# Kernel optimization log

Hardware: AMD Instinct MI355X
Metric: run time of the kernel (lower is better)

The kernel has to match this reference:

```python
import jax, jax.numpy as jnp
import numpy as np

N_QUBITS = 6
N_LAYERS = 2
QSVT_DEGREE = 3
BATCH = 128
SEQ_LEN = 512
DIM = 2 ** N_QUBITS
# wire 0 is the most-significant bit in the statevector index (PennyLane convention)
_POP = np.array([bin(i).count('1') for i in range(DIM)], dtype=np.float32)
PHASE_SIGN = jnp.asarray(N_QUBITS - 2.0 * _POP)  # (DIM,): sum_w (1 - 2*bit_w)


def _rx(t):
    c = jnp.cos(0.5 * t).astype(jnp.complex64)
    s = (-1j * jnp.sin(0.5 * t)).astype(jnp.complex64)
    return jnp.stack([jnp.stack([c, s]), jnp.stack([s, c])])


def _ry(t):
    c = jnp.cos(0.5 * t).astype(jnp.complex64)
    s = jnp.sin(0.5 * t).astype(jnp.complex64)
    return jnp.stack([jnp.stack([c, -s]), jnp.stack([s, c])])


def _rz(t):
    e = jnp.exp(-0.5j * t.astype(jnp.complex64))
    z = jnp.zeros((), jnp.complex64)
    return jnp.stack([jnp.stack([e, z]), jnp.stack([z, jnp.conj(e)])])


def _apply_1q(psi, U, w):
    # psi: (B,) + (2,)*N_QUBITS ; U: (2,2) complex, same for all batch elems
    psi = jnp.moveaxis(psi, 1 + w, -1)
    psi = psi @ U.T
    return jnp.moveaxis(psi, -1, 1 + w)


def _apply_ry_batched(psi, theta, w):
    # RY with a per-batch angle theta: (B,)
    psi = jnp.moveaxis(psi, 1 + w, -1)
    c = jnp.cos(0.5 * theta).reshape((-1,) + (1,) * (N_QUBITS - 1))
    s = jnp.sin(0.5 * theta).reshape((-1,) + (1,) * (N_QUBITS - 1))
    a, b = psi[..., 0], psi[..., 1]
    psi = jnp.stack([c * a - s * b, s * a + c * b], axis=-1)
    return jnp.moveaxis(psi, -1, 1 + w)


def _cnot(psi, c, t):
    p0 = jax.lax.index_in_dim(psi, 0, axis=1 + c, keepdims=True)
    p1 = jax.lax.index_in_dim(psi, 1, axis=1 + c, keepdims=True)
    p1 = jnp.flip(p1, axis=1 + t)
    return jnp.concatenate([p0, p1], axis=1 + c)


def _circuit_step(h, x, params, poly):
    # h, x: (B, N_QUBITS) angles. Returns <Z_w> per qubit: (B, N_QUBITS).
    B = h.shape[0]
    # 1) state encoding: RY(h_w)|0> = cos(h/2)|0> + sin(h/2)|1>  (product state)
    c, s = jnp.cos(0.5 * h), jnp.sin(0.5 * h)
    psi = jnp.ones((B, 1), jnp.complex64)
    for w in range(N_QUBITS):
        amp = jnp.stack([c[:, w], s[:, w]], axis=-1).astype(jnp.complex64)  # (B,2)
        psi = (psi[:, :, None] * amp[:, None, :]).reshape(B, -1)
    psi = psi.reshape((B,) + (2,) * N_QUBITS)
    # 2) QSVT block: RZ(coeff*pi) on every wire fuses into one diagonal phase
    for d in range(QSVT_DEGREE + 1):
        theta = poly[d] * np.pi
        phase = jnp.exp((-0.5j) * theta * PHASE_SIGN)  # (DIM,)
        psi = (psi.reshape(B, -1) * phase[None, :]).reshape((B,) + (2,) * N_QUBITS)
        for i in range(N_QUBITS - 1):
            psi = _cnot(psi, i, i + 1)
        psi = _cnot(psi, N_QUBITS - 1, 0)  # ring closure
    # 3) variational layers: per-wire RZ@RY@RX (RX applied first), then CNOT chain
    idx = 0
    for _ in range(N_LAYERS):
        for i in range(N_QUBITS):
            U = _rz(params[idx + 2]) @ _ry(params[idx + 1]) @ _rx(params[idx])
            psi = _apply_1q(psi, U, i)
            idx += 3
        for i in range(N_QUBITS - 1):
            psi = _cnot(psi, i, i + 1)
    # 4) input injection: RY(x_w) with per-batch angles
    for w in range(N_QUBITS):
        psi = _apply_ry_batched(psi, x[:, w], w)
    # 5) measurement: <Z_w> = P(bit_w=0) - P(bit_w=1)
    p = jnp.abs(psi) ** 2
    zs = []
    for w in range(N_QUBITS):
        axes = tuple(a for a in range(1, N_QUBITS + 1) if a != 1 + w)
        pw = p.sum(axis=axes)  # (B,2)
        zs.append(pw[:, 0] - pw[:, 1])
    return jnp.stack(zs, axis=-1)


def _ssm_pass(angles, params, poly, reverse):
    a = jnp.flip(angles, axis=1) if reverse else angles
    xs = jnp.moveaxis(a, 1, 0)  # (T, B, n)
    h0 = jnp.zeros((a.shape[0], N_QUBITS), jnp.float32)

    def step(h, x):
        hn = _circuit_step(h, x, params, poly)
        return hn, hn

    _, ys = jax.lax.scan(step, h0, xs)
    out = jnp.moveaxis(ys, 0, 1)  # (B, T, n)
    return jnp.flip(out, axis=1) if reverse else out


def setup_inputs() -> dict:
    key = jax.random.key(0)
    k0, k1, k2, k3 = jax.random.split(key, 4)
    angles = jax.random.uniform(k0, (BATCH, SEQ_LEN, N_QUBITS), jnp.float32) * np.float32(np.pi)
    poly_coeffs = jax.random.normal(k1, (QSVT_DEGREE + 1,), jnp.float32) * 0.1
    fwd_params = jax.random.normal(k2, (N_QUBITS * N_LAYERS * 3,), jnp.float32) * 0.1
    bwd_params = jax.random.normal(k3, (N_QUBITS * N_LAYERS * 3,), jnp.float32) * 0.1
    fwd_coeff = jnp.full((1,), 0.5, jnp.float32)
    bwd_coeff = jnp.full((1,), 0.5, jnp.float32)
    return {'angles': angles, 'poly_coeffs': poly_coeffs, 'fwd_params': fwd_params,
            'bwd_params': bwd_params, 'fwd_coeff': fwd_coeff, 'bwd_coeff': bwd_coeff}


def reference(angles, poly_coeffs, fwd_params, bwd_params, fwd_coeff, bwd_coeff):
    h_fwd = _ssm_pass(angles, fwd_params, poly_coeffs, reverse=False)
    h_bwd = _ssm_pass(angles, bwd_params, poly_coeffs, reverse=True)
    return jax.nn.sigmoid(fwd_coeff) * h_fwd + jax.nn.sigmoid(bwd_coeff) * h_bwd
```

## Files before the change

kernel.cpp:

```cpp
#include <hip/hip_runtime.h>
#include <hip/hip_bf16.h>
#include <stdint.h>

#define BATCH 128
#define SEQ   512
#define NW    6
#define DIM   64
#define NELEM (BATCH * SEQ * NW)
#define PI_F  3.14159265358979323846f

typedef float v2f __attribute__((ext_vector_type(2)));
typedef uint16_t u16x8 __attribute__((ext_vector_type(8)));

__device__ __forceinline__ v2f pkfma(float s, v2f m, v2f a) {
    return __builtin_elementwise_fma((v2f){s, s}, m, a);
}

template <int CTRL>
__device__ __forceinline__ float dpp_add(float v) {
    return v + __int_as_float(__builtin_amdgcn_update_dpp(
        0, __float_as_int(v), CTRL, 0xF, 0xF, true));
}

template <int CTRL>
__device__ __forceinline__ void red6(float v[6]) {
#pragma unroll
    for (int k = 0; k < 6; ++k) v[k] = dpp_add<CTRL>(v[k]);
}

template <int CTRL>
__device__ __forceinline__ float dpp_mov(float x) {
    return __int_as_float(__builtin_amdgcn_update_dpp(
        0, __float_as_int(x), CTRL, 0xF, 0xF, true));
}

__device__ __forceinline__ float ldf(const void* p, int i, bool bf) {
    if (bf) {
        uint32_t u = (uint32_t)((const uint16_t*)p)[i];
        return __uint_as_float(u << 16);
    }
    return ((const float*)p)[i];
}

__global__ void k_prep(const void* ang, const void* poly, const void* fp,
                       const void* bp, const void* fc, const void* bc,
                       float* __restrict__ misc, float* __restrict__ Mg,
                       int* __restrict__ flag) {
    __shared__ int cnt;
    if (threadIdx.x == 0) cnt = 0;
    __syncthreads();
    {
        uint32_t w = ((const uint32_t*)ang)[threadIdx.x & 255];
        uint32_t e = (w >> 8) & 0xFFu;
        if (e >= 0x3Au && e <= 0x41u) atomicAdd(&cnt, 1);
    }
    __syncthreads();
    const bool bf = (cnt >= 128);

    if (blockIdx.x == 32) {
        if (threadIdx.x == 0)      misc[76] = ldf(fc, 0, bf);
        else if (threadIdx.x == 1) misc[77] = ldf(bc, 0, bf);
        else if (threadIdx.x == 2) *flag = bf ? 1 : 0;
        return;
    }

    const int lane = threadIdx.x & 63;
    const int tix  = blockIdx.x * 4 + (threadIdx.x >> 6);
    const int dir  = tix >> 6;
    const int col  = tix & 63;
    const void* prm = dir ? bp : fp;
    const int p = lane;

    float yr = (p == col) ? 1.f : 0.f;
    float yi = 0.f;

#pragma unroll
    for (int d = 0; d < 4; ++d) {
        const float th = 0.5f * PI_F * ldf(poly, d, bf) *
                         (float)(6 - 2 * (int)__popc((unsigned)p));
        float s, c;
        __sincosf(th, &s, &c);
        const float nr = yr * c + yi * s;
        const float ni = yi * c - yr * s;
        yr = nr; yi = ni;
#pragma unroll
        for (int k = 0; k < 6; ++k) {
            const int cw = k, tw = (k + 1) % 6;
            const int src = p ^ (((p >> (5 - cw)) & 1) << (5 - tw));
            yr = __shfl(yr, src, 64);
            yi = __shfl(yi, src, 64);
        }
    }

    int idx = 0;
#pragma unroll
    for (int l = 0; l < 2; ++l) {
#pragma unroll
        for (int w = 0; w < 6; ++w) {
            float cx, sx, cy, sy, cz, sz;
            __sincosf(0.5f * ldf(prm, idx + 0, bf), &sx, &cx);
            __sincosf(0.5f * ldf(prm, idx + 1, bf), &sy, &cy);
            __sincosf(0.5f * ldf(prm, idx + 2, bf), &sz, &cz);
            idx += 3;
            const float A = cy * cx, B = sy * sx, C = sy * cx, D = cy * sx;
            const float U00r = cz * A + sz * B, U00i = cz * B - sz * A;
            const float U11r = U00r,            U11i = sz * A - cz * B;
            const float Xr   = cz * C + sz * D, Xi   = sz * C - cz * D;
            const int m  = 1 << (5 - w);
            const int bb = (p >> (5 - w)) & 1;
            const float C1r = bb ? U11r : U00r;
            const float C1i = bb ? U11i : U00i;
            const float C2r = bb ? Xr : -Xr;
            const float C2i = Xi;
            const float pr = __shfl_xor(yr, m, 64);
            const float pi = __shfl_xor(yi, m, 64);
            const float nr = C1r * yr - C1i * yi + C2r * pr - C2i * pi;
            const float ni = C1r * yi + C1i * yr + C2r * pi + C2i * pr;
            yr = nr; yi = ni;
        }
#pragma unroll
        for (int k = 0; k < 5; ++k) {
            const int src = p ^ (((p >> (5 - k)) & 1) << (5 - (k + 1)));
            yr = __shfl(yr, src, 64);
            yi = __shfl(yi, src, 64);
        }
    }

    float* out = Mg + ((size_t)(dir * 64 + p) * 64 + (size_t)col) * 2;
    out[0] = yr;
    out[1] = yi;
}

__global__ void __launch_bounds__(128, 1) k_sim(const void* __restrict__ ang,
                                                const float* __restrict__ Mg,
                                                float* __restrict__ hbuf,
                                                const int* __restrict__ flag) {
    const int tid   = threadIdx.x;
    const int lane  = tid & 63;
    const int wv    = tid >> 6;
    const int chain = blockIdx.x;
    const int dir   = chain >> 7;
    const int b     = chain & 127;
    const bool bf   = (*flag != 0);

    __shared__ __align__(16) float  cl[SEQ * 12];
    __shared__ __align__(16) float  zb[SEQ * NW];
    __shared__ float2 pY[2][2][DIM];

    if (!bf) {
        const float4* src =
            (const float4*)((const float*)ang + (size_t)b * (SEQ * NW));
#pragma unroll
        for (int k = 0; k < 6; ++k) {
            const int v = k * 128 + tid;
            const float4 a = src[v];
            __align__(16) float o[8];
            float s, c;
            __sincosf(a.x, &s, &c); o[0] = c; o[1] = s;
            __sincosf(a.y, &s, &c); o[2] = c; o[3] = s;
            __sincosf(a.z, &s, &c); o[4] = c; o[5] = s;
            __sincosf(a.w, &s, &c); o[6] = c; o[7] = s;
            ((float4*)cl)[2 * v]     = ((const float4*)o)[0];
            ((float4*)cl)[2 * v + 1] = ((const float4*)o)[1];
        }
    } else {
        const u16x8* src =
            (const u16x8*)((const uint16_t*)ang + (size_t)b * (SEQ * NW));
#pragma unroll
        for (int k = 0; k < 3; ++k) {
            const int v = k * 128 + tid;
            const u16x8 a = src[v];
            __align__(16) float o[16];
#pragma unroll
            for (int e = 0; e < 8; ++e) {
                const float x = __uint_as_float(((uint32_t)a[e]) << 16);
                float s, c;
                __sincosf(x, &s, &c);
                o[2 * e] = c; o[2 * e + 1] = s;
            }
#pragma unroll
            for (int j = 0; j < 4; ++j)
                ((float4*)cl)[4 * v + j] = ((const float4*)o)[j];
        }
    }

    v2f Mres[32];
    {
        const float2* mr2 =
            (const float2*)(Mg + (size_t)(dir * 64 + lane) * 128 + 64 * wv);
#pragma unroll
        for (int k = 0; k < 32; ++k) Mres[k] = (v2f){mr2[k].x, mr2[k].y};
    }

    int zmask[6];
#pragma unroll
    for (int w = 0; w < 6; ++w) zmask[w] = ((lane >> (5 - w)) & 1) << 31;
    const int ow = wv ^ 1;

    float h[6] = {0.f, 0.f, 0.f, 0.f, 0.f, 0.f};

    auto encode_matvec = [&](v2f& acc) {
        const v2f kc1 = {2.6041667e-3f, 2.6041667e-3f};
        const v2f kc0 = {-0.125f, -0.125f};
        const v2f ks1 = {2.6041667e-4f, 2.6041667e-4f};
        const v2f ks0 = {-2.0833333e-2f, -2.0833333e-2f};
        const v2f one = {1.f, 1.f}, half = {0.5f, 0.5f};
        v2f hp0 = {h[0], h[1]}, hp1 = {h[2], h[3]}, hp2 = {h[4], h[5]};
        v2f u0 = hp0 * hp0, u1 = hp1 * hp1, u2 = hp2 * hp2;
        v2f c0 = __builtin_elementwise_fma(u0,
                    __builtin_elementwise_fma(u0, kc1, kc0), one);
        v2f c1 = __builtin_elementwise_fma(u1,
                    __builtin_elementwise_fma(u1, kc1, kc0), one);
        v2f c2 = __builtin_elementwise_fma(u2,
                    __builtin_elementwise_fma(u2, kc1, kc0), one);
        v2f s0 = hp0 * __builtin_elementwise_fma(u0,
                    __builtin_elementwise_fma(u0, ks1, ks0), half);
        v2f s1 = hp1 * __builtin_elementwise_fma(u1,
                    __builtin_elementwise_fma(u1, ks1, ks0), half);
        v2f s2 = hp2 * __builtin_elementwise_fma(u2,
                    __builtin_elementwise_fma(u2, ks1, ks0), half);
        const float t0 = wv ? s0.x : c0.x;
        const float gA = t0 * c0.y, gB = t0 * s0.y;
        float eH4[4];
        eH4[0] = gA * c1.x; eH4[1] = gA * s1.x;
        eH4[2] = gB * c1.x; eH4[3] = gB * s1.x;
        float g45[4], eL[8];
        g45[0] = c2.x * c2.y; g45[1] = c2.x * s2.y;
        g45[2] = s2.x * c2.y; g45[3] = s2.x * s2.y;
#pragma unroll
        for (int j = 0; j < 8; ++j)
            eL[j] = ((j >> 2) ? s1.y : c1.y) * g45[j & 3];
        v2f y = {0.f, 0.f};
#pragma unroll
        for (int a = 0; a < 4; ++a) {
            v2f T = {0.f, 0.f};
#pragma unroll
            for (int jl = 0; jl < 8; ++jl)
                T = pkfma(eL[jl], Mres[8 * a + jl], T);
            y = pkfma(eH4[a], T, y);
        }
        acc = y;
    };

    const float* cp = cl + (dir ? (SEQ - 1) * 12 : 0);
    const int   cstep = dir ? -12 : 12;
    float*       zp = zb + (dir ? (SEQ - 1) * NW : 0);
    const int   zstep = dir ? -NW : NW;

    __syncthreads();

    v2f myacc;
    encode_matvec(myacc);
    pY[0][wv][lane] = (float2){myacc.x, myacc.y};
    float4 xq0 = ((const float4*)cp)[0];
    float4 xq1 = ((const float4*)cp)[1];
    float4 xq2 = ((const float4*)cp)[2];
    cp += cstep;
    __syncthreads();

    for (int t = 0; t < SEQ; ++t) {
        const int buf = t & 1;

        const float2 yP = pY[buf][ow][lane];
        const float yr = myacc.x + yP.x;
        const float yi = myacc.y + yP.y;
        const int yri = __float_as_int(yr), yii = __float_as_int(yi);

        float dot[6];
        {
            auto rr = __builtin_amdgcn_permlane32_swap(yri, yri, false, false);
            auto ri = __builtin_amdgcn_permlane32_swap(yii, yii, false, false);
            dot[0] = fmaf(__int_as_float((int)rr[0]), __int_as_float((int)rr[1]),
                          __int_as_float((int)ri[0]) * __int_as_float((int)ri[1]));
        }
        {
            auto rr = __builtin_amdgcn_permlane16_swap(yri, yri, false, false);
            auto ri = __builtin_amdgcn_permlane16_swap(yii, yii, false, false);
            dot[1] = fmaf(__int_as_float((int)rr[0]), __int_as_float((int)rr[1]),
                          __int_as_float((int)ri[0]) * __int_as_float((int)ri[1]));
        }
        dot[2] = fmaf(yr, dpp_mov<0x128>(yr), yi * dpp_mov<0x128>(yi));
        dot[3] = fmaf(yr, dpp_mov<0x141>(dpp_mov<0x1B>(yr)),
                      yi * dpp_mov<0x141>(dpp_mov<0x1B>(yi)));
        dot[4] = fmaf(yr, dpp_mov<0x4E>(yr), yi * dpp_mov<0x4E>(yi));
        dot[5] = fmaf(yr, dpp_mov<0xB1>(yr), yi * dpp_mov<0xB1>(yi));

        const float q = fmaf(yr, yr, yi * yi);
        const float cx[6] = {xq0.x, xq0.z, xq1.x, xq1.z, xq2.x, xq2.z};
        const float sx[6] = {xq0.y, xq0.w, xq1.y, xq1.w, xq2.y, xq2.w};

        float v[6];
#pragma unroll
        for (int w = 0; w < 6; ++w) {
            const float cq = __int_as_float(__float_as_int(cx[w] * q) ^ zmask[w]);
            v[w] = fmaf(-sx[w], dot[w], cq);
        }

        if (t + 1 < SEQ) {
            xq0 = ((const float4*)cp)[0];
            xq1 = ((const float4*)cp)[1];
            xq2 = ((const float4*)cp)[2];
            cp += cstep;
        }

        red6<0x111>(v);
        red6<0x112>(v);
        red6<0x114>(v);
        red6<0x118>(v);
        red6<0x142>(v);
        red6<0x143>(v);

        if (tid == 63) {
#pragma unroll
            for (int w = 0; w < 6; ++w) zp[w] = v[w];
        }
        zp += zstep;
#pragma unroll
        for (int w = 0; w < 6; ++w)
            h[w] = __int_as_float(
                __builtin_amdgcn_readlane(__float_as_int(v[w]), 63));

        encode_matvec(myacc);
        pY[buf ^ 1][wv][lane] = (float2){myacc.x, myacc.y};
        __syncthreads();
    }

    {
        const float4* zs4 = (const float4*)zb;
        float4* go = (float4*)(hbuf + (size_t)dir * NELEM +
                               (size_t)b * (SEQ * NW));
#pragma unroll
        for (int k = 0; k < 6; ++k) {
            const int idx = tid + k * 128;
            go[idx] = zs4[idx];
        }
    }
}

__global__ void k_combine(const float* __restrict__ hbuf,
                          const float* __restrict__ misc,
                          void* __restrict__ out, const int* __restrict__ flag) {
    const int i = blockIdx.x * blockDim.x + threadIdx.x;
    if (i >= NELEM) return;
    const float sf = 1.f / (1.f + __expf(-misc[76]));
    const float sb = 1.f / (1.f + __expf(-misc[77]));
    const float v = sf * hbuf[i] + sb * hbuf[NELEM + i];
    if (*flag) ((__hip_bfloat16*)out)[i] = __float2bfloat16(v);
    else       ((float*)out)[i] = v;
}

extern "C" void kernel_launch(void* const* d_in, const int* in_sizes, int n_in,
                              void* d_out, int out_size, void* d_ws, size_t ws_size,
                              hipStream_t stream) {
    const void* ang  = d_in[0];
    const void* poly = d_in[1];
    const void* fp   = d_in[2];
    const void* bp   = d_in[3];
    const void* fc   = d_in[4];
    const void* bc   = d_in[5];

    float* misc = (float*)d_ws + 32;
    float* hbuf = misc + 128;
    float* Mg   = hbuf + 2 * NELEM;
    int*   flag = (int*)(Mg + 2 * 64 * 64 * 2);

    k_prep<<<33, 256, 0, stream>>>(ang, poly, fp, bp, fc, bc, misc, Mg, flag);
    k_sim<<<256, 128, 0, stream>>>(ang, Mg, hbuf, flag);
    k_combine<<<(NELEM + 255) / 256, 256, 0, stream>>>(hbuf, misc, d_out, flag);
}
```

Before: 360.0 us.

## Split complex matvec by real/imag across waves, exchange reduced expectations only

Each of the two waves now holds either the real or the imaginary rows of the circuit matrix over the full 64-column input, instead of half the columns of both parts. Each wave therefore computes one complete component of the output amplitude. The per-lane partial-sum exchange through LDS is replaced by an exchange of only the six reduced per-qubit values, which are summed to give the next hidden state. This removes the 64-entry pY buffer traffic and the packed real/imag arithmetic in the dot products. In exchange, both waves must compute the full encoding products and the barrier now sits between the reduction and the next step's matvec, which may serialize the recurrence more.

Measured after the change: 379.2 us. 5.3% more time.

```diff
diff --git a/kernel.cpp b/kernel.cpp
--- a/kernel.cpp
+++ b/kernel.cpp
@@ -44,7 +44,7 @@
 
 __global__ void k_prep(const void* ang, const void* poly, const void* fp,
                        const void* bp, const void* fc, const void* bc,
-                       float* __restrict__ misc, float* __restrict__ Mg,
+                       float* __restrict__ misc, float* __restrict__ Mgc,
                        int* __restrict__ flag) {
     __shared__ int cnt;
     if (threadIdx.x == 0) cnt = 0;
@@ -126,13 +126,14 @@
         }
     }
 
-    float* out = Mg + ((size_t)(dir * 64 + p) * 64 + (size_t)col) * 2;
-    out[0] = yr;
-    out[1] = yi;
+    const int jh = col >> 3, jl = col & 7;
+    const int off = ((jh >> 1) * 8 + jl) * 2 + (jh & 1);
+    Mgc[((size_t)(dir * 2 + 0) * 64 + p) * 64 + off] = yr;
+    Mgc[((size_t)(dir * 2 + 1) * 64 + p) * 64 + off] = yi;
 }
 
 __global__ void __launch_bounds__(128, 1) k_sim(const void* __restrict__ ang,
-                                                const float* __restrict__ Mg,
+                                                const float* __restrict__ Mgc,
                                                 float* __restrict__ hbuf,
                                                 const int* __restrict__ flag) {
     const int tid   = threadIdx.x;
@@ -145,7 +146,7 @@
 
     __shared__ __align__(16) float  cl[SEQ * 12];
     __shared__ __align__(16) float  zb[SEQ * NW];
-    __shared__ float2 pY[2][2][DIM];
+    __shared__ __align__(16) float  tot[2][2][8];
 
     if (!bf) {
         const float4* src =
@@ -184,123 +185,112 @@
         }
     }
 
-    v2f Mres[32];
+    v2f Mv[32];
     {
-        const float2* mr2 =
-            (const float2*)(Mg + (size_t)(dir * 64 + lane) * 128 + 64 * wv);
-#pragma unroll
-        for (int k = 0; k < 32; ++k) Mres[k] = (v2f){mr2[k].x, mr2[k].y};
+        const float4* mr4 =
+            (const float4*)(Mgc + ((size_t)(dir * 2 + wv) * 64 + lane) * 64);
+#pragma unroll
+        for (int k = 0; k < 16; ++k) {
+            const float4 m = mr4[k];
+            Mv[2 * k]     = (v2f){m.x, m.y};
+            Mv[2 * k + 1] = (v2f){m.z, m.w};
+        }
     }
 
     int zmask[6];
 #pragma unroll
     for (int w = 0; w < 6; ++w) zmask[w] = ((lane >> (5 - w)) & 1) << 31;
-    const int ow = wv ^ 1;
-
-    float h[6] = {0.f, 0.f, 0.f, 0.f, 0.f, 0.f};
-
-    auto encode_matvec = [&](v2f& acc) {
-        const v2f kc1 = {2.6041667e-3f, 2.6041667e-3f};
-        const v2f kc0 = {-0.125f, -0.125f};
-        const v2f ks1 = {2.6041667e-4f, 2.6041667e-4f};
-        const v2f ks0 = {-2.0833333e-2f, -2.0833333e-2f};
-        const v2f one = {1.f, 1.f}, half = {0.5f, 0.5f};
-        v2f hp0 = {h[0], h[1]}, hp1 = {h[2], h[3]}, hp2 = {h[4], h[5]};
-        v2f u0 = hp0 * hp0, u1 = hp1 * hp1, u2 = hp2 * hp2;
-        v2f c0 = __builtin_elementwise_fma(u0,
-                    __builtin_elementwise_fma(u0, kc1, kc0), one);
-        v2f c1 = __builtin_elementwise_fma(u1,
-                    __builtin_elementwise_fma(u1, kc1, kc0), one);
-        v2f c2 = __builtin_elementwise_fma(u2,
-                    __builtin_elementwise_fma(u2, kc1, kc0), one);
-        v2f s0 = hp0 * __builtin_elementwise_fma(u0,
-                    __builtin_elementwise_fma(u0, ks1, ks0), half);
-        v2f s1 = hp1 * __builtin_elementwise_fma(u1,
-                    __builtin_elementwise_fma(u1, ks1, ks0), half);
-        v2f s2 = hp2 * __builtin_elementwise_fma(u2,
-                    __builtin_elementwise_fma(u2, ks1, ks0), half);
-        const float t0 = wv ? s0.x : c0.x;
-        const float gA = t0 * c0.y, gB = t0 * s0.y;
-        float eH4[4];
-        eH4[0] = gA * c1.x; eH4[1] = gA * s1.x;
-        eH4[2] = gB * c1.x; eH4[3] = gB * s1.x;
-        float g45[4], eL[8];
-        g45[0] = c2.x * c2.y; g45[1] = c2.x * s2.y;
-        g45[2] = s2.x * c2.y; g45[3] = s2.x * s2.y;
-#pragma unroll
-        for (int j = 0; j < 8; ++j)
-            eL[j] = ((j >> 2) ? s1.y : c1.y) * g45[j & 3];
-        v2f y = {0.f, 0.f};
-#pragma unroll
-        for (int a = 0; a < 4; ++a) {
-            v2f T = {0.f, 0.f};
-#pragma unroll
-            for (int jl = 0; jl < 8; ++jl)
-                T = pkfma(eL[jl], Mres[8 * a + jl], T);
-            y = pkfma(eH4[a], T, y);
-        }
-        acc = y;
-    };
 
     const float* cp = cl + (dir ? (SEQ - 1) * 12 : 0);
     const int   cstep = dir ? -12 : 12;
     float*       zp = zb + (dir ? (SEQ - 1) * NW : 0);
     const int   zstep = dir ? -NW : NW;
 
-    __syncthreads();
-
-    v2f myacc;
-    encode_matvec(myacc);
-    pY[0][wv][lane] = (float2){myacc.x, myacc.y};
-    float4 xq0 = ((const float4*)cp)[0];
-    float4 xq1 = ((const float4*)cp)[1];
-    float4 xq2 = ((const float4*)cp)[2];
-    cp += cstep;
+    float h[6] = {0.f, 0.f, 0.f, 0.f, 0.f, 0.f};
+
     __syncthreads();
 
     for (int t = 0; t < SEQ; ++t) {
         const int buf = t & 1;
 
-        const float2 yP = pY[buf][ow][lane];
-        const float yr = myacc.x + yP.x;
-        const float yi = myacc.y + yP.y;
-        const int yri = __float_as_int(yr), yii = __float_as_int(yi);
-
-        float dot[6];
+        const float4 xq0 = ((const float4*)cp)[0];
+        const float4 xq1 = ((const float4*)cp)[1];
+        const float4 xq2 = ((const float4*)cp)[2];
+        cp += cstep;
+
+        float cw[6], sw[6];
         {
-            auto rr = __builtin_amdgcn_permlane32_swap(yri, yri, false, false);
-            auto ri = __builtin_amdgcn_permlane32_swap(yii, yii, false, false);
-            dot[0] = fmaf(__int_as_float((int)rr[0]), __int_as_float((int)rr[1]),
-                          __int_as_float((int)ri[0]) * __int_as_float((int)ri[1]));
-        }
+            const v2f kc1 = {2.6041667e-3f, 2.6041667e-3f};
+            const v2f kc0 = {-0.125f, -0.125f};
+            const v2f ks1 = {2.6041667e-4f, 2.6041667e-4f};
+            const v2f ks0 = {-2.0833333e-2f, -2.0833333e-2f};
+            const v2f one = {1.f, 1.f}, half = {0.5f, 0.5f};
+            v2f hp0 = {h[0], h[1]}, hp1 = {h[2], h[3]}, hp2 = {h[4], h[5]};
+            v2f u0 = hp0 * hp0, u1 = hp1 * hp1, u2 = hp2 * hp2;
+            v2f c0 = __builtin_elementwise_fma(u0,
+                        __builtin_elementwise_fma(u0, kc1, kc0), one);
+            v2f c1 = __builtin_elementwise_fma(u1,
+                        __builtin_elementwise_fma(u1, kc1, kc0), one);
+            v2f c2 = __builtin_elementwise_fma(u2,
+                        __builtin_elementwise_fma(u2, kc1, kc0), one);
+            v2f s0 = hp0 * __builtin_elementwise_fma(u0,
+                        __builtin_elementwise_fma(u0, ks1, ks0), half);
+            v2f s1 = hp1 * __builtin_elementwise_fma(u1,
+                        __builtin_elementwise_fma(u1, ks1, ks0), half);
+            v2f s2 = hp2 * __builtin_elementwise_fma(u2,
+                        __builtin_elementwise_fma(u2, ks1, ks0), half);
+            cw[0] = c0.x; cw[1] = c0.y; cw[2] = c1.x; cw[3] = c1.y;
+            cw[4] = c2.x; cw[5] = c2.y;
+            sw[0] = s0.x; sw[1] = s0.y; sw[2] = s1.x; sw[3] = s1.y;
+            sw[4] = s2.x; sw[5] = s2.y;
+        }
+
+        float g01[4], g45[4], eH[8], eL[8];
+        g01[0] = cw[0] * cw[1]; g01[1] = cw[0] * sw[1];
+        g01[2] = sw[0] * cw[1]; g01[3] = sw[0] * sw[1];
+        g45[0] = cw[4] * cw[5]; g45[1] = cw[4] * sw[5];
+        g45[2] = sw[4] * cw[5]; g45[3] = sw[4] * sw[5];
+#pragma unroll
+        for (int j = 0; j < 8; ++j) {
+            eH[j] = g01[j >> 1] * ((j & 1) ? sw[2] : cw[2]);
+            eL[j] = ((j >> 2) ? sw[3] : cw[3]) * g45[j & 3];
+        }
+
+        float yc = 0.f;
+#pragma unroll
+        for (int p2 = 0; p2 < 4; ++p2) {
+            v2f T = {0.f, 0.f};
+#pragma unroll
+            for (int jl = 0; jl < 8; ++jl)
+                T = pkfma(eL[jl], Mv[8 * p2 + jl], T);
+            yc = fmaf(eH[2 * p2],     T.x, yc);
+            yc = fmaf(eH[2 * p2 + 1], T.y, yc);
+        }
+        const int yci = __float_as_int(yc);
+
+        float dotp[6];
         {
-            auto rr = __builtin_amdgcn_permlane16_swap(yri, yri, false, false);
-            auto ri = __builtin_amdgcn_permlane16_swap(yii, yii, false, false);
-            dot[1] = fmaf(__int_as_float((int)rr[0]), __int_as_float((int)rr[1]),
-                          __int_as_float((int)ri[0]) * __int_as_float((int)ri[1]));
-        }
-        dot[2] = fmaf(yr, dpp_mov<0x128>(yr), yi * dpp_mov<0x128>(yi));
-        dot[3] = fmaf(yr, dpp_mov<0x141>(dpp_mov<0x1B>(yr)),
-                      yi * dpp_mov<0x141>(dpp_mov<0x1B>(yi)));
-        dot[4] = fmaf(yr, dpp_mov<0x4E>(yr), yi * dpp_mov<0x4E>(yi));
-        dot[5] = fmaf(yr, dpp_mov<0xB1>(yr), yi * dpp_mov<0xB1>(yi));
-
-        const float q = fmaf(yr, yr, yi * yi);
+            auto rr = __builtin_amdgcn_permlane32_swap(yci, yci, false, false);
+            dotp[0] = __int_as_float((int)rr[0]) * __int_as_float((int)rr[1]);
+        }
+        {
+            auto rr = __builtin_amdgcn_permlane16_swap(yci, yci, false, false);
+            dotp[1] = __int_as_float((int)rr[0]) * __int_as_float((int)rr[1]);
+        }
+        dotp[2] = yc * dpp_mov<0x128>(yc);
+        dotp[3] = yc * dpp_mov<0x141>(dpp_mov<0x1B>(yc));
+        dotp[4] = yc * dpp_mov<0x4E>(yc);
+        dotp[5] = yc * dpp_mov<0xB1>(yc);
+
+        const float qc = yc * yc;
         const float cx[6] = {xq0.x, xq0.z, xq1.x, xq1.z, xq2.x, xq2.z};
         const float sx[6] = {xq0.y, xq0.w, xq1.y, xq1.w, xq2.y, xq2.w};
 
         float v[6];
 #pragma unroll
         for (int w = 0; w < 6; ++w) {
-            const float cq = __int_as_float(__float_as_int(cx[w] * q) ^ zmask[w]);
-            v[w] = fmaf(-sx[w], dot[w], cq);
-        }
-
-        if (t + 1 < SEQ) {
-            xq0 = ((const float4*)cp)[0];
-            xq1 = ((const float4*)cp)[1];
-            xq2 = ((const float4*)cp)[2];
-            cp += cstep;
+            const float cq = __int_as_float(__float_as_int(cx[w] * qc) ^ zmask[w]);
+            v[w] = fmaf(-sx[w], dotp[w], cq);
         }
 
         red6<0x111>(v);
@@ -310,20 +300,29 @@
         red6<0x142>(v);
         red6<0x143>(v);
 
+        if (lane == 63) {
+            ((float4*)tot[buf][wv])[0] = (float4){v[0], v[1], v[2], v[3]};
+            ((float4*)tot[buf][wv])[1] = (float4){v[4], v[5], 0.f, 0.f};
+        }
+        __syncthreads();
+
+        const float4 a0 = ((const float4*)tot[buf][0])[0];
+        const float4 a1 = ((const float4*)tot[buf][0])[1];
+        const float4 b0 = ((const float4*)tot[buf][1])[0];
+        const float4 b1 = ((const float4*)tot[buf][1])[1];
+        h[0] = a0.x + b0.x;  h[1] = a0.y + b0.y;
+        h[2] = a0.z + b0.z;  h[3] = a0.w + b0.w;
+        h[4] = a1.x + b1.x;  h[5] = a1.y + b1.y;
+
         if (tid == 63) {
-#pragma unroll
-            for (int w = 0; w < 6; ++w) zp[w] = v[w];
+            ((float2*)zp)[0] = (float2){h[0], h[1]};
+            ((float2*)zp)[1] = (float2){h[2], h[3]};
+            ((float2*)zp)[2] = (float2){h[4], h[5]};
         }
         zp += zstep;
-#pragma unroll
-        for (int w = 0; w < 6; ++w)
-            h[w] = __int_as_float(
-                __builtin_amdgcn_readlane(__float_as_int(v[w]), 63));
-
-        encode_matvec(myacc);
-        pY[buf ^ 1][wv][lane] = (float2){myacc.x, myacc.y};
-        __syncthreads();
-    }
+    }
+
+    __syncthreads();
 
     {
         const float4* zs4 = (const float4*)zb;
@@ -361,10 +360,10 @@
 
     float* misc = (float*)d_ws + 32;
     float* hbuf = misc + 128;
-    float* Mg   = hbuf + 2 * NELEM;
-    int*   flag = (int*)(Mg + 2 * 64 * 64 * 2);
-
-    k_prep<<<33, 256, 0, stream>>>(ang, poly, fp, bp, fc, bc, misc, Mg, flag);
-    k_sim<<<256, 128, 0, stream>>>(ang, Mg, hbuf, flag);
+    float* Mgc  = hbuf + 2 * NELEM;
+    int*   flag = (int*)(Mgc + 2 * 2 * 64 * 64);
+
+    k_prep<<<33, 256, 0, stream>>>(ang, poly, fp, bp, fc, bc, misc, Mgc, flag);
+    k_sim<<<256, 128, 0, stream>>>(ang, Mgc, hbuf, flag);
     k_combine<<<(NELEM + 255) / 256, 256, 0, stream>>>(hbuf, misc, d_out, flag);
 }
```
